# Kernel tuning notes

Hardware: AMD Instinct MI355X
Metric: run time of the kernel (lower is better)

The kernel has to match this reference:

```python
import jax, jax.numpy as jnp
import numpy as np

N_HEADS = 16
DIM = 1024
BS, SLEN = 2, 2048
EPS = 1e-12  # F.normalize eps


def setup_inputs() -> dict:
    key = jax.random.key(0)
    ks = jax.random.split(key, 10)
    d = DIM
    inp = {
        "x": jax.random.normal(ks[0], (BS, SLEN, d), dtype=jnp.float32),
        # causal attention mask, as produced by get_masks(causal=True)
        "mask": jnp.tril(jnp.ones((SLEN, SLEN), dtype=bool))[None].repeat(BS, axis=0),
        "Wq": jax.random.normal(ks[1], (d, d), dtype=jnp.float32) / np.sqrt(d),
        "bq": jax.random.normal(ks[2], (d,), dtype=jnp.float32) * 0.02,
        "Wk": jax.random.normal(ks[3], (d, d), dtype=jnp.float32) / np.sqrt(d),
        "bk": jax.random.normal(ks[4], (d,), dtype=jnp.float32) * 0.02,
        "Wv": jax.random.normal(ks[5], (d, d), dtype=jnp.float32) / np.sqrt(d),
        "bv": jax.random.normal(ks[6], (d,), dtype=jnp.float32) * 0.02,
        "Wo": jax.random.normal(ks[7], (d, d), dtype=jnp.float32) / np.sqrt(d),
        "bo": jax.random.normal(ks[8], (d,), dtype=jnp.float32) * 0.02,
        # learnable scale for normalized (cosine) attention
        "attention_scale": jnp.ones((1,), dtype=jnp.float32) / np.sqrt(d // N_HEADS),
    }
    return inp


def _shape(t, bs, h, dph):
    # (bs, len, dim) -> (bs, h, len, dph)
    return t.reshape(bs, -1, h, dph).transpose(0, 2, 1, 3)


def reference(x, mask, Wq, bq, Wk, bk, Wv, bv, Wo, bo, attention_scale):
    bs, qlen, dim = x.shape
    h = N_HEADS
    dph = dim // h

    q = _shape(x @ Wq + bq, bs, h, dph)  # (bs, h, qlen, dph)
    k = _shape(x @ Wk + bk, bs, h, dph)
    v = _shape(x @ Wv + bv, bs, h, dph)

    # normalized (cosine) attention: L2-normalize q and k, learned scale
    q = q / jnp.maximum(jnp.linalg.norm(q, axis=-1, keepdims=True), EPS)
    k = k / jnp.maximum(jnp.linalg.norm(k, axis=-1, keepdims=True), EPS)
    q = q * attention_scale

    scores = jnp.einsum("bhqd,bhkd->bhqk", q, k)  # (bs, h, qlen, klen)
    scores = jnp.where(mask[:, None, :, :], scores, -jnp.inf)
    weights = jax.nn.softmax(scores, axis=-1)

    ctx = jnp.einsum("bhqk,bhkd->bhqd", weights, v)
    ctx = ctx.transpose(0, 2, 1, 3).reshape(bs, qlen, dim)
    return ctx @ Wo + bo
```

## Files before the change

### kernel.cpp

```cpp
#include <hip/hip_runtime.h>
#include <math.h>

#define NH 16
#define DPH 64
#define SLEN 2048
#define BSZ 2
#define DIM 1024
#define NTOK (BSZ * SLEN)
#define LOG2E 1.44269504088896f

typedef unsigned short ushortT;
typedef __attribute__((ext_vector_type(8))) short short8;
typedef __attribute__((ext_vector_type(4))) short s16x4;
typedef __attribute__((ext_vector_type(4))) float f32x4;

typedef __attribute__((address_space(1))) const unsigned int gu32c;
typedef __attribute__((address_space(3))) unsigned int lu32;

__device__ __forceinline__ void gld16(const void* g, void* l) {
    __builtin_amdgcn_global_load_lds((gu32c*)g, (lu32*)l, 16, 0, 0);
}

__device__ __forceinline__ ushortT f2bf(float f) {
    unsigned int u = __builtin_bit_cast(unsigned int, f);
    u = u + 0x7fffu + ((u >> 16) & 1u);
    return (ushortT)(u >> 16);
}

__global__ __launch_bounds__(256) void cvt_all(const float* __restrict__ x,
                                               ushortT* __restrict__ xb,
                                               const float* __restrict__ W0, const float* __restrict__ W1,
                                               const float* __restrict__ W2, const float* __restrict__ W3,
                                               ushortT* __restrict__ T0, ushortT* __restrict__ T1,
                                               ushortT* __restrict__ T2, ushortT* __restrict__ T3) {
    __shared__ float tile[64][65];
    const int tid = threadIdx.x;
    const int bid = blockIdx.x;
    if (bid < 2048) {
        size_t i = (size_t)bid * 256 + tid;
        float4 a = *(const float4*)&x[i * 8];
        float4 b = *(const float4*)&x[i * 8 + 4];
        short8 v;
        v[0] = (short)f2bf(a.x); v[1] = (short)f2bf(a.y);
        v[2] = (short)f2bf(a.z); v[3] = (short)f2bf(a.w);
        v[4] = (short)f2bf(b.x); v[5] = (short)f2bf(b.y);
        v[6] = (short)f2bf(b.z); v[7] = (short)f2bf(b.w);
        *(short8*)&xb[i * 8] = v;
        return;
    }
    const int widx = bid - 2048;
    const int z = widx >> 8, rem = widx & 255;
    const float* W = z == 0 ? W0 : z == 1 ? W1 : z == 2 ? W2 : W3;
    ushortT* T = z == 0 ? T0 : z == 1 ? T1 : z == 2 ? T2 : T3;
    const int kb = (rem >> 4) * 64, nb = (rem & 15) * 64;
#pragma unroll
    for (int it = 0; it < 4; it++) {
        int chunk = it * 256 + tid;
        int r = chunk >> 4, c4 = (chunk & 15) * 4;
        *(float4*)&tile[r][c4] = *(const float4*)&W[(size_t)(kb + r) * DIM + nb + c4];
    }
    __syncthreads();
#pragma unroll
    for (int it = 0; it < 2; it++) {
        int chunk = it * 256 + tid;
        int n = chunk >> 3, k8 = (chunk & 7) * 8;
        short8 o;
#pragma unroll
        for (int j = 0; j < 8; j++) o[j] = (short)f2bf(tile[k8 + j][n]);
        *(short8*)&T[(size_t)(nb + n) * DIM + kb + k8] = o;
    }
}

__global__ __launch_bounds__(512, 2) void gemm_qkv8(const ushortT* __restrict__ A,
                                                    const ushortT* __restrict__ Bt,
                                                    const float* __restrict__ bq,
                                                    const float* __restrict__ bk,
                                                    const float* __restrict__ bv,
                                                    const float* __restrict__ ascale,
                                                    ushortT* __restrict__ Qb,
                                                    ushortT* __restrict__ Kb,
                                                    ushortT* __restrict__ VF) {
    __shared__ __align__(16) ushortT lds[65536];
    const int tid = threadIdx.x;
    const int lane = tid & 63, wid = tid >> 6;
    const int wm = wid >> 2, wn = wid & 3;
    const int lo = lane & 15, hi = lane >> 4;
    const int bid = blockIdx.x;
    const int swz = (bid & 7) * 24 + (bid >> 3);
    const int bx = swz % 12, by = swz / 12;
    const int row0 = by * 256, col0 = bx * 256;
    const int srow2 = tid >> 2, sc = tid & 3;
    f32x4 acc[8][4] = {};
    short8 af[4], bfr[4];

    auto stage = [&](int isA, int buf, int ksh, int kt) {
        const ushortT* g = isA ? A : Bt;
        int r0 = isA ? row0 : col0;
        int base = (isA ? 0 : 32768) + (buf * 2 + ksh) * 8192;
#pragma unroll
        for (int r = 0; r < 2; r++) {
            int rl = r * 128 + srow2;
            int gch = sc ^ ((rl >> 1) & 3);
            gld16(&g[(size_t)(r0 + rl) * DIM + kt * 64 + ksh * 32 + gch * 8],
                  &lds[base + r * 4096 + tid * 8]);
        }
    };
    auto loadA = [&](int buf, int ks, int mh) {
        int base = (buf * 2 + ks) * 8192;
#pragma unroll
        for (int mm = 0; mm < 4; mm++) {
            int row = wm * 128 + (mh * 4 + mm) * 16 + lo;
            af[mm] = *(const short8*)&lds[base + row * 32 + (hi ^ ((row >> 1) & 3)) * 8];
        }
    };
    auto loadB = [&](int buf, int ks) {
        int base = 32768 + (buf * 2 + ks) * 8192;
#pragma unroll
        for (int n = 0; n < 4; n++) {
            int row = wn * 64 + n * 16 + lo;
            bfr[n] = *(const short8*)&lds[base + row * 32 + (hi ^ ((row >> 1) & 3)) * 8];
        }
    };
    auto mfma16 = [&](int mh) {
        __builtin_amdgcn_s_setprio(1);
#pragma unroll
        for (int mm = 0; mm < 4; mm++)
#pragma unroll
            for (int n = 0; n < 4; n++)
                acc[mh * 4 + mm][n] = __builtin_amdgcn_mfma_f32_16x16x32_bf16(
                    af[mm], bfr[n], acc[mh * 4 + mm][n], 0, 0, 0);
        __builtin_amdgcn_s_setprio(0);
    };

    stage(0, 0, 0, 0); stage(1, 0, 0, 0);
    stage(0, 0, 1, 0); stage(1, 0, 1, 0);
    asm volatile("s_waitcnt vmcnt(4)" ::: "memory");
    asm volatile("s_barrier" ::: "memory");

#pragma unroll 1
    for (int it = 0; it < 8; ++it) {
        const int e = it * 2, o = e + 1;
        const bool more = (it < 7);
        loadA(0, 0, 0); loadB(0, 0);
        stage(0, 1, 0, o); stage(1, 1, 0, o);
        asm volatile("s_barrier" ::: "memory");
        mfma16(0);
        asm volatile("s_waitcnt vmcnt(4)" ::: "memory");
        asm volatile("s_barrier" ::: "memory");
        loadA(0, 0, 1);
        asm volatile("s_barrier" ::: "memory");
        mfma16(1);
        asm volatile("s_barrier" ::: "memory");
        loadA(0, 1, 0); loadB(0, 1);
        stage(0, 1, 1, o); stage(1, 1, 1, o);
        asm volatile("s_barrier" ::: "memory");
        mfma16(0);
        asm volatile("s_waitcnt vmcnt(4)" ::: "memory");
        asm volatile("s_barrier" ::: "memory");
        loadA(0, 1, 1);
        asm volatile("s_barrier" ::: "memory");
        mfma16(1);
        asm volatile("s_barrier" ::: "memory");
        loadA(1, 0, 0); loadB(1, 0);
        if (more) { stage(0, 0, 0, e + 2); stage(1, 0, 0, e + 2); }
        asm volatile("s_barrier" ::: "memory");
        mfma16(0);
        if (more) { asm volatile("s_waitcnt vmcnt(4)" ::: "memory"); }
        else      { asm volatile("s_waitcnt vmcnt(0)" ::: "memory"); }
        asm volatile("s_barrier" ::: "memory");
        loadA(1, 0, 1);
        asm volatile("s_barrier" ::: "memory");
        mfma16(1);
        asm volatile("s_barrier" ::: "memory");
        loadA(1, 1, 0); loadB(1, 1);
        if (more) { stage(0, 0, 1, e + 2); stage(1, 0, 1, e + 2); }
        asm volatile("s_barrier" ::: "memory");
        mfma16(0);
        if (more) { asm volatile("s_waitcnt vmcnt(4)" ::: "memory"); }
        asm volatile("s_barrier" ::: "memory");
        loadA(1, 1, 1);
        asm volatile("s_barrier" ::: "memory");
        mfma16(1);
        asm volatile("s_barrier" ::: "memory");
    }
    __syncthreads();

    const int cg = col0 + wn * 64;
    const int which = cg >> 10;
    const int cwin = cg & 1023;
    const int h = cwin >> 6;
    const int t0g = row0 + wm * 128;
    const int b = t0g >> 11, tok0 = t0g & (SLEN - 1);
    const float* bias = which == 0 ? bq : which == 1 ? bk : bv;

    float bb4[4];
#pragma unroll
    for (int n = 0; n < 4; n++) bb4[n] = bias[cwin + n * 16 + lo];
#pragma unroll
    for (int m = 0; m < 8; m++)
#pragma unroll
        for (int n = 0; n < 4; n++)
#pragma unroll
            for (int r = 0; r < 4; r++) acc[m][n][r] += bb4[n];

    if (which < 2) {
        float asc = (which == 0) ? ascale[0] * LOG2E : 1.0f;
#pragma unroll
        for (int m = 0; m < 8; m++)
#pragma unroll
            for (int r = 0; r < 4; r++) {
                float ss = acc[m][0][r] * acc[m][0][r] + acc[m][1][r] * acc[m][1][r] +
                           acc[m][2][r] * acc[m][2][r] + acc[m][3][r] * acc[m][3][r];
#pragma unroll
                for (int o = 8; o > 0; o >>= 1) ss += __shfl_xor(ss, o);
                float sc2 = asc / fmaxf(sqrtf(ss), 1e-12f);
#pragma unroll
                for (int n = 0; n < 4; n++) acc[m][n][r] *= sc2;
            }
    }

    ushortT* tl = &lds[wid * 8192];
    if (which < 2) {
#pragma unroll
        for (int m = 0; m < 8; m++)
#pragma unroll
            for (int n = 0; n < 4; n++)
#pragma unroll
                for (int r = 0; r < 4; r++) {
                    int row = m * 16 + 4 * hi + r;
                    int c = n * 2 + (lo >> 3);
                    tl[row * 64 + ((c ^ (row & 7)) << 3) + (lo & 7)] = f2bf(acc[m][n][r]);
                }
        ushortT* op = which == 0 ? Qb : Kb;
        const size_t base = ((size_t)(b * NH + h) * SLEN + tok0) * DPH;
#pragma unroll
        for (int j = 0; j < 16; j++) {
            int cid = j * 64 + lane;
            int rowL = cid >> 3, c = cid & 7;
            uint4 v = *(const uint4*)&tl[rowL * 64 + ((c ^ (rowL & 7)) << 3)];
            *(uint4*)&op[base + (size_t)cid * 8] = v;
        }
    } else {
#pragma unroll
        for (int m = 0; m < 8; m++)
#pragma unroll
            for (int n = 0; n < 4; n++)
#pragma unroll
                for (int r = 0; r < 4; r++) {
                    int row = m * 16 + 4 * hi + r;
                    int c = n * 2 + (lo >> 3);
                    tl[row * 64 + ((c ^ ((row >> 3) & 7)) << 3) + (lo & 7)] = f2bf(acc[m][n][r]);
                }
        const int bh = b * NH + h;
        const int kt0 = tok0 >> 6;
#pragma unroll
        for (int i = 0; i < 16; i++) {
            int kk = i >> 3;
            int c = i & 7;
            int jd = c >> 1, ks2 = c & 1;
            int colL = jd * 16 + lo;
            int c2 = colL >> 3;
            short8 v;
#pragma unroll
            for (int e2 = 0; e2 < 8; e2++) {
                int rowL = kk * 64 + ks2 * 32 + 8 * hi + e2;
                v[e2] = (short)tl[rowL * 64 + ((c2 ^ ((rowL >> 3) & 7)) << 3) + (colL & 7)];
            }
            *(short8*)&VF[((size_t)bh * 32 + kt0 + kk) * 4096 + (size_t)(c * 64 + lane) * 8] = v;
        }
    }
}

__global__ __launch_bounds__(256) void gemm_oproj(const ushortT* __restrict__ A,
                                                  const ushortT* __restrict__ Bt,
                                                  const float* __restrict__ bias,
                                                  float* __restrict__ outF) {
    __shared__ __align__(16) ushortT lds[32768];
    const int tid = threadIdx.x;
    const int lane = tid & 63, wid = tid >> 6;
    const int wr = wid >> 1, wc = wid & 1;
    const int lo = lane & 15, hi = lane >> 4;
    const int bid = blockIdx.x;
    const int swz = (bid & 7) * 32 + (bid >> 3);
    const int bx = swz & 7, by = swz >> 3;
    const int row0 = by * 128, col0 = bx * 128;
    f32x4 acc[4][4] = {};
    short8 afO[4], bfO[4];

    auto stageO = [&](int isA, int slot, int kh) {
        const ushortT* g = isA ? A : Bt;
        int r0 = isA ? row0 : col0;
        int base = (isA ? 0 : 16384) + slot * 4096;
#pragma unroll
        for (int r = 0; r < 2; r++) {
            int ch = r * 256 + tid;
            int row = ch >> 2, kc = ch & 3;
            gld16(&g[(size_t)(r0 + row) * DIM + kh * 32 + (kc ^ ((row >> 1) & 3)) * 8],
                  &lds[base + r * 2048 + tid * 8]);
        }
    };
    auto loadAO = [&](int slot) {
        int base = slot * 4096;
#pragma unroll
        for (int m = 0; m < 4; m++) {
            int row = wr * 64 + m * 16 + lo;
            afO[m] = *(const short8*)&lds[base + row * 32 + (hi ^ ((row >> 1) & 3)) * 8];
        }
    };
    auto loadBO = [&](int slot) {
        int base = 16384 + slot * 4096;
#pragma unroll
        for (int n = 0; n < 4; n++) {
            int row = wc * 64 + n * 16 + lo;
            bfO[n] = *(const short8*)&lds[base + row * 32 + (hi ^ ((row >> 1) & 3)) * 8];
        }
    };
    auto mfmaO = [&]() {
        __builtin_amdgcn_s_setprio(1);
#pragma unroll
        for (int m = 0; m < 4; m++)
#pragma unroll
            for (int n = 0; n < 4; n++)
                acc[m][n] = __builtin_amdgcn_mfma_f32_16x16x32_bf16(afO[m], bfO[n], acc[m][n], 0, 0, 0);
        __builtin_amdgcn_s_setprio(0);
    };

    stageO(0, 0, 0); stageO(1, 0, 0);
    stageO(0, 1, 1); stageO(1, 1, 1);
    stageO(0, 2, 2); stageO(1, 2, 2);
    asm volatile("s_waitcnt vmcnt(8)" ::: "memory");
    asm volatile("s_barrier" ::: "memory");

#pragma unroll 1
    for (int it = 0; it < 8; ++it) {
        const int k0 = it * 4;
        const bool last = (it == 7);
        loadAO(0); loadBO(0);
        stageO(0, 3, k0 + 3); stageO(1, 3, k0 + 3);
        asm volatile("s_barrier" ::: "memory");
        mfmaO();
        asm volatile("s_waitcnt vmcnt(8)" ::: "memory");
        asm volatile("s_barrier" ::: "memory");
        loadAO(1); loadBO(1);
        if (!last) { stageO(0, 0, k0 + 4); stageO(1, 0, k0 + 4); }
        asm volatile("s_barrier" ::: "memory");
        mfmaO();
        if (!last) { asm volatile("s_waitcnt vmcnt(8)" ::: "memory"); }
        else       { asm volatile("s_waitcnt vmcnt(4)" ::: "memory"); }
        asm volatile("s_barrier" ::: "memory");
        loadAO(2); loadBO(2);
        if (!last) { stageO(0, 1, k0 + 5); stageO(1, 1, k0 + 5); }
        asm volatile("s_barrier" ::: "memory");
        mfmaO();
        if (!last) { asm volatile("s_waitcnt vmcnt(8)" ::: "memory"); }
        else       { asm volatile("s_waitcnt vmcnt(0)" ::: "memory"); }
        asm volatile("s_barrier" ::: "memory");
        loadAO(3); loadBO(3);
        if (!last) { stageO(0, 2, k0 + 6); stageO(1, 2, k0 + 6); }
        asm volatile("s_barrier" ::: "memory");
        mfmaO();
        if (!last) { asm volatile("s_waitcnt vmcnt(8)" ::: "memory"); }
        asm volatile("s_barrier" ::: "memory");
    }
    __syncthreads();

    float bb[4];
#pragma unroll
    for (int n = 0; n < 4; n++) bb[n] = bias[col0 + wc * 64 + n * 16 + lo];
#pragma unroll
    for (int m = 0; m < 4; m++)
#pragma unroll
        for (int n = 0; n < 4; n++)
#pragma unroll
            for (int r = 0; r < 4; r++) acc[m][n][r] += bb[n];

    float* tl = (float*)lds + wid * 4096;
#pragma unroll
    for (int m = 0; m < 4; m++)
#pragma unroll
        for (int n = 0; n < 4; n++)
#pragma unroll
            for (int r = 0; r < 4; r++) {
                int row = m * 16 + hi * 4 + r;
                int col = n * 16 + lo;
                int cc = col >> 2;
                tl[row * 64 + ((cc ^ (row & 7)) << 2) + (col & 3)] = acc[m][n][r];
            }
#pragma unroll
    for (int j = 0; j < 16; j++) {
        int cid = j * 64 + lane;
        int rowR = cid >> 4, cc = cid & 15;
        f32x4 v = *(const f32x4*)&tl[rowR * 64 + ((cc ^ (rowR & 7)) << 2)];
        int rg = row0 + wr * 64 + rowR;
        int cgl = col0 + wc * 64 + cc * 4;
        *(f32x4*)&outF[(size_t)rg * DIM + cgl] = v;
    }
}

__global__ __launch_bounds__(512, 4) void attn(const ushortT* __restrict__ Q,
                                               const ushortT* __restrict__ K,
                                               const ushortT* __restrict__ VF,
                                               const float* __restrict__ scale,
                                               ushortT* __restrict__ ctx) {
    __shared__ __align__(16) ushortT Ks[64 * 64];
    __shared__ __align__(16) ushortT Ps[8 * 16 * 64];
    const int tid = threadIdx.x, lane = tid & 63, wid = tid >> 6;
    const int wg = wid & 3, sg = wid >> 2;
    const int bh = blockIdx.x, p = blockIdx.y;
    const int qt = sg ? p : 31 - p;
    const int kbmax = 31 - p;
    const size_t hb = (size_t)bh * SLEN * DPH;
    const int lo = lane & 15, hi = lane >> 4;
    const float mshift = fabsf(scale[0]) * LOG2E;

    short8 aq[2];
    {
        const int qrow = qt * 64 + wg * 16 + lo;
#pragma unroll
        for (int ks = 0; ks < 2; ks++)
            aq[ks] = *(const short8*)&Q[hb + (size_t)qrow * DPH + ks * 32 + 8 * hi];
    }

    const int srow = tid >> 3, sslot = tid & 7;
    const int sldsoff = srow * 64 + ((sslot ^ (srow & 7)) << 3);
    uint4 kr = *(const uint4*)&K[hb + (size_t)srow * DPH + sslot * 8];
    *(uint4*)&Ks[sldsoff] = kr;
    __syncthreads();

    f32x4 accd[4] = {};
    float lp = 0.f;

    for (int kb = 0; kb <= kbmax; kb++) {
        if (kb < kbmax)
            kr = *(const uint4*)&K[hb + (size_t)((kb + 1) * 64 + srow) * DPH + sslot * 8];

        if (kb <= qt) {
            short8 bv[8];
            const ushortT* vt = &VF[(((size_t)bh * 32 + kb) * 512 + lane) * 8];
#pragma unroll
            for (int c = 0; c < 8; c++) bv[c] = *(const short8*)&vt[(size_t)c * 512];

            f32x4 sf[4] = {};
#pragma unroll
            for (int ks = 0; ks < 2; ks++)
#pragma unroll
                for (int j = 0; j < 4; j++) {
                    int row = j * 16 + lo;
                    short8 bk = *(const short8*)&Ks[row * 64 + (((ks * 4 + hi) ^ (row & 7)) << 3)];
                    sf[j] = __builtin_amdgcn_mfma_f32_16x16x32_bf16(bk, aq[ks], sf[j], 0, 0, 0);
                }

            if (kb == qt) {
#pragma unroll
                for (int j = 0; j < 4; j++)
#pragma unroll
                    for (int r = 0; r < 4; r++)
                        if (j * 16 + 4 * hi + r > wg * 16 + lo) sf[j][r] = -INFINITY;
            }

#pragma unroll
            for (int j = 0; j < 4; j++) {
                s16x4 pk;
#pragma unroll
                for (int r = 0; r < 4; r++) {
                    float pv = __builtin_amdgcn_exp2f(sf[j][r] - mshift);
                    lp += pv;
                    pk[r] = (short)f2bf(pv);
                }
                int slot = (4 * j + hi) ^ (2 * (lo & 7));
                *(s16x4*)&Ps[wid * 1024 + lo * 64 + slot * 4] = pk;
            }

#pragma unroll
            for (int ks = 0; ks < 2; ks++) {
                int slot0 = (8 * ks + 2 * hi) ^ (2 * (lo & 7));
                short8 ap = *(const short8*)&Ps[wid * 1024 + lo * 64 + slot0 * 4];
#pragma unroll
                for (int jd = 0; jd < 4; jd++)
                    accd[jd] = __builtin_amdgcn_mfma_f32_16x16x32_bf16(ap, bv[jd * 2 + ks], accd[jd], 0, 0, 0);
            }
        }

        __syncthreads();
        if (kb < kbmax) {
            *(uint4*)&Ks[sldsoff] = kr;
            __syncthreads();
        }
    }

    lp += __shfl_xor(lp, 16);
    lp += __shfl_xor(lp, 32);

    const int b = bh >> 4, h = bh & 15;
#pragma unroll
    for (int r = 0; r < 4; r++) {
        float lr = __shfl(lp, (lane & 48) | (4 * hi + r));
        float inv = 1.0f / lr;
        int t = qt * 64 + wg * 16 + 4 * hi + r;
#pragma unroll
        for (int jd = 0; jd < 4; jd++) {
            int d = jd * 16 + lo;
            ctx[(size_t)(b * SLEN + t) * DIM + h * 64 + d] = f2bf(accd[jd][r] * inv);
        }
    }
}

extern "C" void kernel_launch(void* const* d_in, const int* in_sizes, int n_in,
                              void* d_out, int out_size, void* d_ws,
                              size_t ws_size, hipStream_t stream) {
    const float* x = (const float*)d_in[0];
    const float* Wq = (const float*)d_in[2];
    const float* bq = (const float*)d_in[3];
    const float* Wk = (const float*)d_in[4];
    const float* bk = (const float*)d_in[5];
    const float* Wv = (const float*)d_in[6];
    const float* bv = (const float*)d_in[7];
    const float* Wo = (const float*)d_in[8];
    const float* bo = (const float*)d_in[9];
    const float* ascale = (const float*)d_in[10];
    float* outF = (float*)d_out;

    unsigned char* ws = (unsigned char*)d_ws;
    const size_t MB = 1u << 20;
    ushortT* xb = (ushortT*)(ws);
    ushortT* Wqkvt = (ushortT*)(ws + 8 * MB);
    ushortT* Wot = (ushortT*)(ws + 14 * MB);
    ushortT* Qb = (ushortT*)(ws + 16 * MB);
    ushortT* Kb = (ushortT*)(ws + 24 * MB);
    ushortT* VFb = (ushortT*)(ws + 32 * MB);
    ushortT* ctxb = (ushortT*)(ws + 40 * MB);

    cvt_all<<<3072, 256, 0, stream>>>(x, xb, Wq, Wk, Wv, Wo, Wqkvt,
                                      Wqkvt + (size_t)1024 * 1024,
                                      Wqkvt + (size_t)2048 * 1024, Wot);

    gemm_qkv8<<<dim3(192), 512, 0, stream>>>(xb, Wqkvt, bq, bk, bv, ascale, Qb, Kb, VFb);

    attn<<<dim3(32, 16), 512, 0, stream>>>(Qb, Kb, VFb, ascale, ctxb);

    gemm_oproj<<<dim3(256), 256, 0, stream>>>(ctxb, Wot, bo, outF);
}
```

Measured before the change: 106.4 us.

## Deepen QKV GEMM prefetch pipeline and cut barriers per k-step

Restructures the QKV projection GEMM main loop to prefetch more stages ahead, interleaving individual stage loads between MFMA half-blocks and waiting with vmcnt(8) instead of vmcnt(4). Several barriers are removed, so each sub-step now has one barrier instead of two. The aim is to hide global-to-LDS load latency better and reduce synchronisation stalls. In exchange it raises the number of loads in flight and relies on precise buffer-reuse ordering, which risks LDS races if the reduced barriers turn out insufficient.

```diff
diff --git a/kernel.cpp b/kernel.cpp
--- a/kernel.cpp
+++ b/kernel.cpp
@@ -132,56 +132,52 @@
         __builtin_amdgcn_s_setprio(0);
     };
 
-    stage(0, 0, 0, 0); stage(1, 0, 0, 0);
-    stage(0, 0, 1, 0); stage(1, 0, 1, 0);
-    asm volatile("s_waitcnt vmcnt(4)" ::: "memory");
-    asm volatile("s_barrier" ::: "memory");
+    stage(1, 0, 0, 0); stage(0, 0, 0, 0);
+    stage(1, 0, 1, 0); stage(0, 0, 1, 0);
+    stage(1, 1, 0, 1); stage(0, 1, 0, 1);
 
 #pragma unroll 1
     for (int it = 0; it < 8; ++it) {
-        const int e = it * 2, o = e + 1;
+        const int o = it * 2 + 1;
         const bool more = (it < 7);
+        asm volatile("s_waitcnt vmcnt(8)" ::: "memory");
+        asm volatile("s_barrier" ::: "memory");
         loadA(0, 0, 0); loadB(0, 0);
-        stage(0, 1, 0, o); stage(1, 1, 0, o);
-        asm volatile("s_barrier" ::: "memory");
+        stage(1, 1, 1, o);
         mfma16(0);
-        asm volatile("s_waitcnt vmcnt(4)" ::: "memory");
         asm volatile("s_barrier" ::: "memory");
         loadA(0, 0, 1);
-        asm volatile("s_barrier" ::: "memory");
+        stage(0, 1, 1, o);
         mfma16(1);
+        asm volatile("s_waitcnt vmcnt(8)" ::: "memory");
         asm volatile("s_barrier" ::: "memory");
         loadA(0, 1, 0); loadB(0, 1);
-        stage(0, 1, 1, o); stage(1, 1, 1, o);
-        asm volatile("s_barrier" ::: "memory");
+        if (more) stage(1, 0, 0, o + 1);
         mfma16(0);
-        asm volatile("s_waitcnt vmcnt(4)" ::: "memory");
         asm volatile("s_barrier" ::: "memory");
         loadA(0, 1, 1);
-        asm volatile("s_barrier" ::: "memory");
+        if (more) stage(0, 0, 0, o + 1);
         mfma16(1);
+        if (more) { asm volatile("s_waitcnt vmcnt(8)" ::: "memory"); }
+        else      { asm volatile("s_waitcnt vmcnt(4)" ::: "memory"); }
         asm volatile("s_barrier" ::: "memory");
         loadA(1, 0, 0); loadB(1, 0);
-        if (more) { stage(0, 0, 0, e + 2); stage(1, 0, 0, e + 2); }
-        asm volatile("s_barrier" ::: "memory");
+        if (more) stage(1, 0, 1, o + 1);
         mfma16(0);
-        if (more) { asm volatile("s_waitcnt vmcnt(4)" ::: "memory"); }
+        asm volatile("s_barrier" ::: "memory");
+        loadA(1, 0, 1);
+        if (more) stage(0, 0, 1, o + 1);
+        mfma16(1);
+        if (more) { asm volatile("s_waitcnt vmcnt(8)" ::: "memory"); }
         else      { asm volatile("s_waitcnt vmcnt(0)" ::: "memory"); }
         asm volatile("s_barrier" ::: "memory");
-        loadA(1, 0, 1);
-        asm volatile("s_barrier" ::: "memory");
+        loadA(1, 1, 0); loadB(1, 1);
+        if (more) stage(1, 1, 0, o + 2);
+        mfma16(0);
+        asm volatile("s_barrier" ::: "memory");
+        loadA(1, 1, 1);
+        if (more) stage(0, 1, 0, o + 2);
         mfma16(1);
-        asm volatile("s_barrier" ::: "memory");
-        loadA(1, 1, 0); loadB(1, 1);
-        if (more) { stage(0, 0, 1, e + 2); stage(1, 0, 1, e + 2); }
-        asm volatile("s_barrier" ::: "memory");
-        mfma16(0);
-        if (more) { asm volatile("s_waitcnt vmcnt(4)" ::: "memory"); }
-        asm volatile("s_barrier" ::: "memory");
-        loadA(1, 1, 1);
-        asm volatile("s_barrier" ::: "memory");
-        mfma16(1);
-        asm volatile("s_barrier" ::: "memory");
     }
     __syncthreads();
 
@@ -262,9 +258,9 @@
             int c2 = colL >> 3;
             short8 v;
 #pragma unroll
-            for (int e2 = 0; e2 < 8; e2++) {
-                int rowL = kk * 64 + ks2 * 32 + 8 * hi + e2;
-                v[e2] = (short)tl[rowL * 64 + ((c2 ^ ((rowL >> 3) & 7)) << 3) + (colL & 7)];
+            for (int e = 0; e < 8; e++) {
+                int rowL = kk * 64 + ks2 * 32 + 8 * hi + e;
+                v[e] = (short)tl[rowL * 64 + ((c2 ^ ((rowL >> 3) & 7)) << 3) + (colL & 7)];
             }
             *(short8*)&VF[((size_t)bh * 32 + kt0 + kk) * 4096 + (size_t)(c * 64 + lane) * 8] = v;
         }
```

Result: faster. 98.49 us (-7.4%).
